# Kernel optimization log

Measured on AMD Instinct MI355X. Metric: run time of the kernel, lower is better.

## Reference

```python
import jax, jax.numpy as jnp
import numpy as np

B, S, DM, NH, DK, DFF = 4, 2048, 512, 8, 64, 2048
EPS = 1e-5


def setup_inputs() -> dict:
    key = jax.random.key(0)
    ks = jax.random.split(key, 16)
    sd = 1.0 / np.sqrt(DM)
    inp = {
        'x': jax.random.normal(ks[0], (B, S, DM), dtype=jnp.float32),
        'wq': jax.random.normal(ks[1], (DM, DM), dtype=jnp.float32) * sd,
        'bq': jnp.zeros((DM,), dtype=jnp.float32),
        'wk': jax.random.normal(ks[2], (DM, DM), dtype=jnp.float32) * sd,
        'bk': jnp.zeros((DM,), dtype=jnp.float32),
        'wv': jax.random.normal(ks[3], (DM, DM), dtype=jnp.float32) * sd,
        'bv': jnp.zeros((DM,), dtype=jnp.float32),
        'wo': jax.random.normal(ks[4], (DM, DM), dtype=jnp.float32) * sd,
        'bo': jnp.zeros((DM,), dtype=jnp.float32),
        'ln_g': jnp.ones((DM,), dtype=jnp.float32),
        'ln_b': jnp.zeros((DM,), dtype=jnp.float32),
        'w1': jax.random.normal(ks[5], (DFF, DM), dtype=jnp.float32) * sd,
        'b1': jnp.zeros((DFF,), dtype=jnp.float32),
        'w2': jax.random.normal(ks[6], (DM, DFF), dtype=jnp.float32) * (1.0 / np.sqrt(DFF)),
        'b2': jnp.zeros((DM,), dtype=jnp.float32),
    }
    return inp


def _layernorm(x, g, b):
    mu = jnp.mean(x, axis=-1, keepdims=True)
    var = jnp.mean(jnp.square(x - mu), axis=-1, keepdims=True)
    return (x - mu) * jax.lax.rsqrt(var + EPS) * g + b


def reference(x, wq, bq, wk, bk, wv, bv, wo, bo, ln_g, ln_b, w1, b1, w2, b2):
    # projections (torch Linear: y = x @ W.T + b)
    q = x @ wq.T + bq
    k = x @ wk.T + bk
    v = x @ wv.T + bv
    # chunk along feature dim into NH heads of size DK
    q = q.reshape(B, S, NH, DK)
    k = k.reshape(B, S, NH, DK)
    v = v.reshape(B, S, NH, DK)
    scores = jnp.einsum('bihd,bjhd->bhij', q, k) / np.sqrt(DK)  # [B,NH,S,S]
    probs = jax.nn.softmax(scores, axis=-1)
    o = jnp.einsum('bhij,bjhd->bihd', probs, v).reshape(B, S, DM)
    o = o @ wo.T + bo
    # residual + shared layernorm (dropout p=0 -> identity)
    h = _layernorm(o + x, ln_g, ln_b)
    ff = jax.nn.relu(h @ w1.T + b1) @ w2.T + b2
    return _layernorm(ff + h, ln_g, ln_b)
```

## Files before the change

### kernel.cpp

```cpp
#include <hip/hip_runtime.h>

typedef __attribute__((ext_vector_type(8))) short short8;
typedef __attribute__((ext_vector_type(8))) unsigned short ushort8;
typedef __attribute__((ext_vector_type(4))) unsigned short ushort4v;
typedef __attribute__((ext_vector_type(4))) float f32x4;
typedef __attribute__((ext_vector_type(16))) float f32x16;

#define DEV static __device__ __forceinline__

DEV unsigned short f2bf(float f) {
  unsigned u = __builtin_bit_cast(unsigned, f);
  u += 0x7fffu + ((u >> 16) & 1u);
  return (unsigned short)(u >> 16);
}

DEV float bf2f(unsigned short u) {
  return __builtin_bit_cast(float, (unsigned)u << 16);
}

DEV void gload_lds16(const void* g, void* l) {
  __builtin_amdgcn_global_load_lds((__attribute__((address_space(1))) void*)g,
                                   (__attribute__((address_space(3))) void*)l,
                                   16, 0, 0);
}

DEV unsigned cvtpk(float lo, float hi) {
  unsigned u;
  asm("v_cvt_pk_bf16_f32 %0, %1, %2" : "=v"(u) : "v"(lo), "v"(hi));
  return u;
}

DEV void pl32(unsigned& a, unsigned& b) {
  asm("v_permlane32_swap_b32 %0, %1" : "+v"(a), "+v"(b));
}

DEV short8 pack4(unsigned a, unsigned b, unsigned c, unsigned d) {
  int4 t = make_int4((int)a, (int)b, (int)c, (int)d);
  return __builtin_bit_cast(short8, t);
}

__global__ __launch_bounds__(256) void cvt_all_k(
    const float4* __restrict__ wq, const float4* __restrict__ wk,
    const float4* __restrict__ wv, const float4* __restrict__ wo,
    const float4* __restrict__ w1, const float4* __restrict__ w2,
    const float4* __restrict__ x, ushort4v* __restrict__ wqkv,
    ushort4v* __restrict__ wob, ushort4v* __restrict__ w1b,
    ushort4v* __restrict__ w2b, ushort4v* __restrict__ xb) {
  const int i = threadIdx.x;
  const int b = blockIdx.x;
  const float4* s;
  ushort4v* d;
  size_t u;
  if (b < 256)       { s = wq; d = wqkv;          u = (size_t)b * 256 + i; }
  else if (b < 512)  { s = wk; d = wqkv + 65536;  u = (size_t)(b - 256) * 256 + i; }
  else if (b < 768)  { s = wv; d = wqkv + 131072; u = (size_t)(b - 512) * 256 + i; }
  else if (b < 1024) { s = wo; d = wob;           u = (size_t)(b - 768) * 256 + i; }
  else if (b < 2048) { s = w1; d = w1b;           u = (size_t)(b - 1024) * 256 + i; }
  else if (b < 3072) { s = w2; d = w2b;           u = (size_t)(b - 2048) * 256 + i; }
  else               { s = x;  d = xb;            u = (size_t)(b - 3072) * 256 + i; }
  float4 v = s[u];
  ushort4v o = { f2bf(v.x), f2bf(v.y), f2bf(v.z), f2bf(v.w) };
  d[u] = o;
}

__global__ void pack_bias_k(const float* __restrict__ bq, const float* __restrict__ bk,
                            const float* __restrict__ bv, float* __restrict__ o) {
  int i = threadIdx.x;
  o[i] = bq[i];
  o[512 + i] = bk[i];
  o[1024 + i] = bv[i];
}

template <int EPI>
__global__ __launch_bounds__(256) void gemm_bt(
    const unsigned short* __restrict__ A, const unsigned short* __restrict__ Bw,
    const float* __restrict__ bias, int M, int N, int K,
    unsigned short* __restrict__ outb, float* __restrict__ outf,
    const unsigned short* __restrict__ residb) {
  __shared__ __align__(16) unsigned short As[128 * 64];
  __shared__ __align__(16) unsigned short Bs[128 * 64];
  const int tid = threadIdx.x;
  const int lane = tid & 63;
  const int wv = tid >> 6;
  const int wr = wv >> 1, wc = wv & 1;
  const int lrow = lane & 15, lgrp = lane >> 4;
  const int bm = blockIdx.x * 128;
  const int bn = blockIdx.y * 128;

  f32x4 acc[4][4];
#pragma unroll
  for (int m = 0; m < 4; m++)
#pragma unroll
    for (int n = 0; n < 4; n++) acc[m][n] = (f32x4){0.f, 0.f, 0.f, 0.f};

  for (int k0 = 0; k0 < K; k0 += 64) {
    __syncthreads();
#pragma unroll
    for (int i = 0; i < 4; i++) {
      const int sb = wv * 64 + i * 256;
      const int slot = sb + lane;
      const int row = slot >> 3;
      const int cc = (slot & 7) ^ (row & 7);
      gload_lds16(A + (size_t)(bm + row) * K + k0 + cc * 8, &As[sb * 8]);
      gload_lds16(Bw + (size_t)(bn + row) * K + k0 + cc * 8, &Bs[sb * 8]);
    }
    __syncthreads();

#pragma unroll
    for (int kk = 0; kk < 2; kk++) {
      short8 af[4], bfr[4];
#pragma unroll
      for (int m = 0; m < 4; m++) {
        const int row = wr * 64 + m * 16 + lrow;
        af[m] = *(const short8*)&As[row * 64 + (((lgrp + 4 * kk) ^ (row & 7)) * 8)];
      }
#pragma unroll
      for (int n = 0; n < 4; n++) {
        const int row = wc * 64 + n * 16 + lrow;
        bfr[n] = *(const short8*)&Bs[row * 64 + (((lgrp + 4 * kk) ^ (row & 7)) * 8)];
      }
#pragma unroll
      for (int m = 0; m < 4; m++)
#pragma unroll
        for (int n = 0; n < 4; n++)
          acc[m][n] = __builtin_amdgcn_mfma_f32_16x16x32_bf16(af[m], bfr[n], acc[m][n], 0, 0, 0);
    }
  }

  if constexpr (EPI == 0) {
    const int proj = bn >> 9;
    if (proj == 2) {
      __shared__ __align__(16) unsigned short VT[128 * 136];
#pragma unroll
      for (int n = 0; n < 4; n++) {
        const int cl = wc * 64 + n * 16 + lrow;
        const float bval = bias[bn + cl];
#pragma unroll
        for (int m = 0; m < 4; m++)
#pragma unroll
          for (int r = 0; r < 4; r++)
            VT[cl * 136 + wr * 64 + m * 16 + lgrp * 4 + r] = f2bf(acc[m][n][r] + bval);
      }
      __syncthreads();
      const int j = (bn - 1024) >> 7;
      const int b = bm >> 11;
      const int sbase = bm & 2047;
      unsigned short* vout = outb + (size_t)2 * 4194304;
#pragma unroll
      for (int q = 0; q < 8; q++) {
        const int chunk = q * 256 + tid;
        const int cl = chunk >> 4, s8 = chunk & 15;
        const int head = 2 * j + (cl >> 6), d = cl & 63;
        ushort8 val = *(const ushort8*)&VT[cl * 136 + s8 * 8];
        *(ushort8*)(vout + ((size_t)(b * 8 + head) * 64 + d) * 2048 + sbase + s8 * 8) = val;
      }
    } else {
      const float qs = (proj == 0) ? 0.18033688011f : 1.0f;
#pragma unroll
      for (int m = 0; m < 4; m++) {
#pragma unroll
        for (int n = 0; n < 4; n++) {
          const int gcol = bn + wc * 64 + n * 16 + lrow;
          const float bval = bias[gcol];
          const int feat = gcol & 511;
          const int head = feat >> 6, d = feat & 63;
#pragma unroll
          for (int r = 0; r < 4; r++) {
            const int grow = bm + wr * 64 + m * 16 + lgrp * 4 + r;
            const int b = grow >> 11, s = grow & 2047;
            const int bh = b * 8 + head;
            outb[(size_t)proj * 4194304 + ((size_t)bh * 2048 + s) * 64 + d] =
                f2bf((acc[m][n][r] + bval) * qs);
          }
        }
      }
    }
  } else {
#pragma unroll
    for (int m = 0; m < 4; m++) {
#pragma unroll
      for (int n = 0; n < 4; n++) {
        const int gcol = bn + wc * 64 + n * 16 + lrow;
        const float bval = bias[gcol];
#pragma unroll
        for (int r = 0; r < 4; r++) {
          const int grow = bm + wr * 64 + m * 16 + lgrp * 4 + r;
          float v = acc[m][n][r] + bval;
          const size_t o = (size_t)grow * N + gcol;
          if constexpr (EPI == 1) {
            outb[o] = f2bf(v + bf2f(residb[o]));
          } else if constexpr (EPI == 2) {
            outb[o] = f2bf(v > 0.f ? v : 0.f);
          } else {
            outf[o] = v + bf2f(residb[o]);
          }
        }
      }
    }
  }
}

template <int EPI>
__global__ __launch_bounds__(256) void gemm_n64(
    const unsigned short* __restrict__ A, const unsigned short* __restrict__ Bw,
    const float* __restrict__ bias, int M, int N, int K,
    unsigned short* __restrict__ outb, float* __restrict__ outf,
    const unsigned short* __restrict__ residb) {
  __shared__ __align__(16) unsigned short As[128 * 64];
  __shared__ __align__(16) unsigned short Bs[64 * 64];
  const int tid = threadIdx.x;
  const int lane = tid & 63;
  const int wv = tid >> 6;
  const int lrow = lane & 15, lgrp = lane >> 4;
  const int bm = blockIdx.x * 128;
  const int bn = blockIdx.y * 64;

  f32x4 acc[2][4];
#pragma unroll
  for (int m = 0; m < 2; m++)
#pragma unroll
    for (int n = 0; n < 4; n++) acc[m][n] = (f32x4){0.f, 0.f, 0.f, 0.f};

  for (int k0 = 0; k0 < K; k0 += 64) {
    __syncthreads();
#pragma unroll
    for (int i = 0; i < 4; i++) {
      const int sb = wv * 64 + i * 256;
      const int slot = sb + lane;
      const int row = slot >> 3;
      const int cc = (slot & 7) ^ (row & 7);
      gload_lds16(A + (size_t)(bm + row) * K + k0 + cc * 8, &As[sb * 8]);
    }
#pragma unroll
    for (int i = 0; i < 2; i++) {
      const int sb = wv * 64 + i * 256;
      const int slot = sb + lane;
      const int row = slot >> 3;
      const int cc = (slot & 7) ^ (row & 7);
      gload_lds16(Bw + (size_t)(bn + row) * K + k0 + cc * 8, &Bs[sb * 8]);
    }
    __syncthreads();

#pragma unroll
    for (int kk = 0; kk < 2; kk++) {
      short8 af[2], bfr[4];
#pragma unroll
      for (int m = 0; m < 2; m++) {
        const int row = wv * 32 + m * 16 + lrow;
        af[m] = *(const short8*)&As[row * 64 + (((lgrp + 4 * kk) ^ (row & 7)) * 8)];
      }
#pragma unroll
      for (int n = 0; n < 4; n++) {
        const int row = n * 16 + lrow;
        bfr[n] = *(const short8*)&Bs[row * 64 + (((lgrp + 4 * kk) ^ (row & 7)) * 8)];
      }
#pragma unroll
      for (int m = 0; m < 2; m++)
#pragma unroll
        for (int n = 0; n < 4; n++)
          acc[m][n] = __builtin_amdgcn_mfma_f32_16x16x32_bf16(af[m], bfr[n], acc[m][n], 0, 0, 0);
    }
  }

#pragma unroll
  for (int m = 0; m < 2; m++) {
#pragma unroll
    for (int n = 0; n < 4; n++) {
      const int gcol = bn + n * 16 + lrow;
      const float bval = bias[gcol];
#pragma unroll
      for (int r = 0; r < 4; r++) {
        const int grow = bm + wv * 32 + m * 16 + lgrp * 4 + r;
        float v = acc[m][n][r] + bval;
        const size_t o = (size_t)grow * N + gcol;
        if constexpr (EPI == 1) {
          outb[o] = f2bf(v + bf2f(residb[o]));
        } else {
          outf[o] = v + bf2f(residb[o]);
        }
      }
    }
  }
}

__global__ __launch_bounds__(256) void attn_k(
    const unsigned short* __restrict__ Qg, const unsigned short* __restrict__ Kg,
    const unsigned short* __restrict__ Vg, unsigned short* __restrict__ Og) {
  __shared__ __align__(16) unsigned short Kl[2][128 * 64];
  __shared__ __align__(16) unsigned short Vl[2][64 * 128];
  const int tid = threadIdx.x, lane = tid & 63, wq = tid >> 6;
  const int ql = lane & 31;
  const int hi = lane >> 5;
  const int bid = blockIdx.x;
  const int lin = (bid & 7) * 64 + (bid >> 3);
  const int bh = lin >> 4;
  const int q0 = (lin & 15) * 128;
  const int qw = q0 + wq * 32;
  const size_t hbase = (size_t)bh * (2048 * 64);

  int kR[4], kC[4], vR[4], vC[4];
#pragma unroll
  for (int i = 0; i < 4; i++) {
    const int slot = i * 256 + tid;
    kR[i] = slot >> 3;
    kC[i] = (slot & 7) ^ (kR[i] & 7);
    vR[i] = slot >> 4;
    vC[i] = (slot & 15) ^ (vR[i] & 15);
  }

  short8 qreg[4];
  {
    const unsigned short* qp = Qg + hbase + (size_t)(qw + ql) * 64 + hi * 8;
#pragma unroll
    for (int i = 0; i < 4; i++) qreg[i] = *(const short8*)(qp + 16 * i);
  }

  f32x16 oac0 = {0.f, 0.f, 0.f, 0.f, 0.f, 0.f, 0.f, 0.f,
                 0.f, 0.f, 0.f, 0.f, 0.f, 0.f, 0.f, 0.f};
  f32x16 oac1 = oac0;
  float lr = 0.f;

#pragma unroll
  for (int i = 0; i < 4; i++) {
    const int db = (i * 256 + wq * 64) * 8;
    gload_lds16(Kg + hbase + (size_t)kR[i] * 64 + kC[i] * 8, &Kl[0][db]);
    gload_lds16(Vg + hbase + (size_t)vR[i] * 2048 + vC[i] * 8, &Vl[0][db]);
  }
  __syncthreads();

  for (int it = 0; it < 16; ++it) {
    const int cur = it & 1;
    if (it < 15) {
      const int kt = (it + 1) * 128;
      const int nxt = cur ^ 1;
#pragma unroll
      for (int i = 0; i < 4; i++) {
        const int db = (i * 256 + wq * 64) * 8;
        gload_lds16(Kg + hbase + (size_t)(kt + kR[i]) * 64 + kC[i] * 8, &Kl[nxt][db]);
        gload_lds16(Vg + hbase + (size_t)vR[i] * 2048 + kt + vC[i] * 8, &Vl[nxt][db]);
      }
    }

#pragma unroll
    for (int hf = 0; hf < 2; hf++) {
      f32x16 sc0 = {0.f, 0.f, 0.f, 0.f, 0.f, 0.f, 0.f, 0.f,
                    0.f, 0.f, 0.f, 0.f, 0.f, 0.f, 0.f, 0.f};
      f32x16 sc1 = sc0;
      __builtin_amdgcn_s_setprio(1);
#pragma unroll
      for (int i = 0; i < 4; i++) {
        const int c8 = 2 * i + hi;
        const int r0 = hf * 64 + ql;
        const int r1 = hf * 64 + ql + 32;
        short8 ka = *(const short8*)&Kl[cur][(r0 * 8 + (c8 ^ (r0 & 7))) * 8];
        short8 kb = *(const short8*)&Kl[cur][(r1 * 8 + (c8 ^ (r1 & 7))) * 8];
        sc0 = __builtin_amdgcn_mfma_f32_32x32x16_bf16(ka, qreg[i], sc0, 0, 0, 0);
        sc1 = __builtin_amdgcn_mfma_f32_32x32x16_bf16(kb, qreg[i], sc1, 0, 0, 0);
      }
      __builtin_amdgcn_s_setprio(0);

      short8 pa[4];
#pragma unroll
      for (int t2 = 0; t2 < 2; t2++) {
        const f32x16& sc = t2 ? sc1 : sc0;
        float p[16];
#pragma unroll
        for (int r = 0; r < 16; r++) {
          p[r] = __builtin_amdgcn_exp2f(sc[r]);
          lr += p[r];
        }
        unsigned w0a = cvtpk(p[0], p[1]),   w0b = cvtpk(p[2], p[3]);
        unsigned w1a = cvtpk(p[4], p[5]),   w1b = cvtpk(p[6], p[7]);
        unsigned w2a = cvtpk(p[8], p[9]),   w2b = cvtpk(p[10], p[11]);
        unsigned w3a = cvtpk(p[12], p[13]), w3b = cvtpk(p[14], p[15]);
        pl32(w0a, w1a);
        pl32(w0b, w1b);
        pa[2 * t2] = pack4(w0a, w0b, w1a, w1b);
        pl32(w2a, w3a);
        pl32(w2b, w3b);
        pa[2 * t2 + 1] = pack4(w2a, w2b, w3a, w3b);
      }

      __builtin_amdgcn_s_setprio(1);
#pragma unroll
      for (int ks = 0; ks < 4; ks++) {
        const int c8 = hf * 8 + 2 * ks + hi;
        const int r0 = ql;
        const int r1 = ql + 32;
        short8 vb0 = *(const short8*)&Vl[cur][(r0 * 16 + (c8 ^ (r0 & 15))) * 8];
        short8 vb1 = *(const short8*)&Vl[cur][(r1 * 16 + (c8 ^ (r1 & 15))) * 8];
        oac0 = __builtin_amdgcn_mfma_f32_32x32x16_bf16(pa[ks], vb0, oac0, 0, 0, 0);
        oac1 = __builtin_amdgcn_mfma_f32_32x32x16_bf16(pa[ks], vb1, oac1, 0, 0, 0);
      }
      __builtin_amdgcn_s_setprio(0);
    }

    __syncthreads();
  }

  lr += __shfl_xor(lr, 32);
  const float inv = 1.0f / lr;

  const int b = bh >> 3, h = bh & 7;
#pragma unroll
  for (int r = 0; r < 16; r++) {
    const int qrow = (r & 3) + 8 * (r >> 2) + 4 * hi;
    const float invr = __shfl(inv, qrow);
    const size_t base = ((size_t)(b * 2048 + qw + qrow)) * 512 + h * 64 + ql;
    Og[base] = f2bf(oac0[r] * invr);
    Og[base + 32] = f2bf(oac1[r] * invr);
  }
}

__global__ __launch_bounds__(64) void ln_k(const float* __restrict__ in,
                                           const float* __restrict__ g,
                                           const float* __restrict__ bb,
                                           float* __restrict__ outf) {
  const int row = blockIdx.x, lane = threadIdx.x;
  const float4* p = (const float4*)(in + (size_t)row * 512);
  float4 a = p[lane], b4 = p[lane + 64];
  float s = a.x + a.y + a.z + a.w + b4.x + b4.y + b4.z + b4.w;
#pragma unroll
  for (int off = 32; off >= 1; off >>= 1) s += __shfl_xor(s, off);
  const float mu = s * (1.f / 512.f);
  float q = 0.f;
  {
    float d;
    d = a.x - mu; q += d * d; d = a.y - mu; q += d * d;
    d = a.z - mu; q += d * d; d = a.w - mu; q += d * d;
    d = b4.x - mu; q += d * d; d = b4.y - mu; q += d * d;
    d = b4.z - mu; q += d * d; d = b4.w - mu; q += d * d;
  }
#pragma unroll
  for (int off = 32; off >= 1; off >>= 1) q += __shfl_xor(q, off);
  const float rstd = rsqrtf(q * (1.f / 512.f) + 1e-5f);
  const float4* gp = (const float4*)g;
  const float4* bp = (const float4*)bb;
  float4 g0 = gp[lane], g1 = gp[lane + 64], c0 = bp[lane], c1 = bp[lane + 64];
  float4 o0, o1;
  o0.x = (a.x - mu) * rstd * g0.x + c0.x;
  o0.y = (a.y - mu) * rstd * g0.y + c0.y;
  o0.z = (a.z - mu) * rstd * g0.z + c0.z;
  o0.w = (a.w - mu) * rstd * g0.w + c0.w;
  o1.x = (b4.x - mu) * rstd * g1.x + c1.x;
  o1.y = (b4.y - mu) * rstd * g1.y + c1.y;
  o1.z = (b4.z - mu) * rstd * g1.z + c1.z;
  o1.w = (b4.w - mu) * rstd * g1.w + c1.w;
  float4* of = (float4*)(outf + (size_t)row * 512);
  of[lane] = o0;
  of[lane + 64] = o1;
}

__global__ __launch_bounds__(64) void ln_bf_k(const unsigned short* __restrict__ in,
                                              const float* __restrict__ g,
                                              const float* __restrict__ bb,
                                              unsigned short* __restrict__ out) {
  const int row = blockIdx.x, lane = threadIdx.x;
  ushort8 v = *(const ushort8*)(in + (size_t)row * 512 + lane * 8);
  float f[8];
#pragma unroll
  for (int j = 0; j < 8; j++) f[j] = bf2f(v[j]);
  float s = 0.f;
#pragma unroll
  for (int j = 0; j < 8; j++) s += f[j];
#pragma unroll
  for (int off = 32; off >= 1; off >>= 1) s += __shfl_xor(s, off);
  const float mu = s * (1.f / 512.f);
  float q = 0.f;
#pragma unroll
  for (int j = 0; j < 8; j++) { const float d = f[j] - mu; q += d * d; }
#pragma unroll
  for (int off = 32; off >= 1; off >>= 1) q += __shfl_xor(q, off);
  const float rstd = rsqrtf(q * (1.f / 512.f) + 1e-5f);
  const float4* gp = (const float4*)g;
  const float4* bp = (const float4*)bb;
  float4 g0 = gp[lane * 2], g1 = gp[lane * 2 + 1];
  float4 c0 = bp[lane * 2], c1 = bp[lane * 2 + 1];
  const float gg[8] = {g0.x, g0.y, g0.z, g0.w, g1.x, g1.y, g1.z, g1.w};
  const float cc[8] = {c0.x, c0.y, c0.z, c0.w, c1.x, c1.y, c1.z, c1.w};
  ushort8 ov;
#pragma unroll
  for (int j = 0; j < 8; j++) ov[j] = f2bf((f[j] - mu) * rstd * gg[j] + cc[j]);
  *(ushort8*)(out + (size_t)row * 512 + lane * 8) = ov;
}

extern "C" void kernel_launch(void* const* d_in, const int* in_sizes, int n_in,
                              void* d_out, int out_size, void* d_ws, size_t ws_size,
                              hipStream_t stream) {
  const float* x = (const float*)d_in[0];
  const float* wq = (const float*)d_in[1];
  const float* bq = (const float*)d_in[2];
  const float* wk = (const float*)d_in[3];
  const float* bk = (const float*)d_in[4];
  const float* wv = (const float*)d_in[5];
  const float* bv = (const float*)d_in[6];
  const float* wo = (const float*)d_in[7];
  const float* bo = (const float*)d_in[8];
  const float* ln_g = (const float*)d_in[9];
  const float* ln_b = (const float*)d_in[10];
  const float* w1 = (const float*)d_in[11];
  const float* b1 = (const float*)d_in[12];
  const float* w2 = (const float*)d_in[13];
  const float* b2 = (const float*)d_in[14];

  unsigned short* ws_u = (unsigned short*)d_ws;
  unsigned short* wqkv = ws_u;
  unsigned short* wob = wqkv + 786432;
  unsigned short* w1b = wob + 262144;
  unsigned short* w2b = w1b + 1048576;
  unsigned short* xb = w2b + 1048576;
  unsigned short* qb = xb + 4194304;
  unsigned short* kb = qb + 4194304;
  unsigned short* vtb = kb + 4194304;
  unsigned short* ob = vtb + 4194304;
  unsigned short* s1b = ob + 4194304;
  unsigned short* hb = s1b + 4194304;
  unsigned short* f1b = qb;
  float* bqkv = (float*)(hb + 4194304);

  cvt_all_k<<<7168, 256, 0, stream>>>(
      (const float4*)wq, (const float4*)wk, (const float4*)wv, (const float4*)wo,
      (const float4*)w1, (const float4*)w2, (const float4*)x,
      (ushort4v*)wqkv, (ushort4v*)wob, (ushort4v*)w1b, (ushort4v*)w2b,
      (ushort4v*)xb);
  pack_bias_k<<<1, 512, 0, stream>>>(bq, bk, bv, bqkv);

  gemm_bt<0><<<dim3(64, 12), 256, 0, stream>>>(xb, wqkv, bqkv, 8192, 1536, 512,
                                               qb, nullptr, nullptr);
  attn_k<<<512, 256, 0, stream>>>(qb, kb, vtb, ob);
  gemm_n64<1><<<dim3(64, 8), 256, 0, stream>>>(ob, wob, bo, 8192, 512, 512,
                                               s1b, nullptr, xb);
  ln_bf_k<<<8192, 64, 0, stream>>>(s1b, ln_g, ln_b, hb);
  gemm_bt<2><<<dim3(64, 16), 256, 0, stream>>>(hb, w1b, b1, 8192, 2048, 512,
                                               f1b, nullptr, nullptr);
  gemm_n64<3><<<dim3(64, 8), 256, 0, stream>>>(f1b, w2b, b2, 8192, 512, 2048,
                                               nullptr, (float*)d_out, hb);
  ln_k<<<8192, 64, 0, stream>>>((float*)d_out, ln_g, ln_b, (float*)d_out);
}
```

Measured before the change: 166.4 us.

## Compute softmax row sums via MFMA and store FFN residual output as bf16

```diff
diff --git a/kernel.cpp b/kernel.cpp
--- a/kernel.cpp
+++ b/kernel.cpp
@@ -315,10 +315,13 @@
     for (int i = 0; i < 4; i++) qreg[i] = *(const short8*)(qp + 16 * i);
   }
 
+  const unsigned one2 = 0x3F803F80u;
+  const short8 ones = pack4(one2, one2, one2, one2);
+
   f32x16 oac0 = {0.f, 0.f, 0.f, 0.f, 0.f, 0.f, 0.f, 0.f,
                  0.f, 0.f, 0.f, 0.f, 0.f, 0.f, 0.f, 0.f};
   f32x16 oac1 = oac0;
-  float lr = 0.f;
+  f32x16 lacc = oac0;
 
 #pragma unroll
   for (int i = 0; i < 4; i++) {
@@ -365,10 +368,7 @@
         const f32x16& sc = t2 ? sc1 : sc0;
         float p[16];
 #pragma unroll
-        for (int r = 0; r < 16; r++) {
-          p[r] = __builtin_amdgcn_exp2f(sc[r]);
-          lr += p[r];
-        }
+        for (int r = 0; r < 16; r++) p[r] = __builtin_amdgcn_exp2f(sc[r]);
         unsigned w0a = cvtpk(p[0], p[1]),   w0b = cvtpk(p[2], p[3]);
         unsigned w1a = cvtpk(p[4], p[5]),   w1b = cvtpk(p[6], p[7]);
         unsigned w2a = cvtpk(p[8], p[9]),   w2b = cvtpk(p[10], p[11]);
@@ -391,64 +391,23 @@
         short8 vb1 = *(const short8*)&Vl[cur][(r1 * 16 + (c8 ^ (r1 & 15))) * 8];
         oac0 = __builtin_amdgcn_mfma_f32_32x32x16_bf16(pa[ks], vb0, oac0, 0, 0, 0);
         oac1 = __builtin_amdgcn_mfma_f32_32x32x16_bf16(pa[ks], vb1, oac1, 0, 0, 0);
+        lacc = __builtin_amdgcn_mfma_f32_32x32x16_bf16(pa[ks], ones, lacc, 0, 0, 0);
       }
       __builtin_amdgcn_s_setprio(0);
     }
 
     __syncthreads();
   }
-
-  lr += __shfl_xor(lr, 32);
-  const float inv = 1.0f / lr;
 
   const int b = bh >> 3, h = bh & 7;
 #pragma unroll
   for (int r = 0; r < 16; r++) {
     const int qrow = (r & 3) + 8 * (r >> 2) + 4 * hi;
-    const float invr = __shfl(inv, qrow);
+    const float invr = 1.0f / lacc[r];
     const size_t base = ((size_t)(b * 2048 + qw + qrow)) * 512 + h * 64 + ql;
     Og[base] = f2bf(oac0[r] * invr);
     Og[base + 32] = f2bf(oac1[r] * invr);
   }
-}
-
-__global__ __launch_bounds__(64) void ln_k(const float* __restrict__ in,
-                                           const float* __restrict__ g,
-                                           const float* __restrict__ bb,
-                                           float* __restrict__ outf) {
-  const int row = blockIdx.x, lane = threadIdx.x;
-  const float4* p = (const float4*)(in + (size_t)row * 512);
-  float4 a = p[lane], b4 = p[lane + 64];
-  float s = a.x + a.y + a.z + a.w + b4.x + b4.y + b4.z + b4.w;
-#pragma unroll
-  for (int off = 32; off >= 1; off >>= 1) s += __shfl_xor(s, off);
-  const float mu = s * (1.f / 512.f);
-  float q = 0.f;
-  {
-    float d;
-    d = a.x - mu; q += d * d; d = a.y - mu; q += d * d;
-    d = a.z - mu; q += d * d; d = a.w - mu; q += d * d;
-    d = b4.x - mu; q += d * d; d = b4.y - mu; q += d * d;
-    d = b4.z - mu; q += d * d; d = b4.w - mu; q += d * d;
-  }
-#pragma unroll
-  for (int off = 32; off >= 1; off >>= 1) q += __shfl_xor(q, off);
-  const float rstd = rsqrtf(q * (1.f / 512.f) + 1e-5f);
-  const float4* gp = (const float4*)g;
-  const float4* bp = (const float4*)bb;
-  float4 g0 = gp[lane], g1 = gp[lane + 64], c0 = bp[lane], c1 = bp[lane + 64];
-  float4 o0, o1;
-  o0.x = (a.x - mu) * rstd * g0.x + c0.x;
-  o0.y = (a.y - mu) * rstd * g0.y + c0.y;
-  o0.z = (a.z - mu) * rstd * g0.z + c0.z;
-  o0.w = (a.w - mu) * rstd * g0.w + c0.w;
-  o1.x = (b4.x - mu) * rstd * g1.x + c1.x;
-  o1.y = (b4.y - mu) * rstd * g1.y + c1.y;
-  o1.z = (b4.z - mu) * rstd * g1.z + c1.z;
-  o1.w = (b4.w - mu) * rstd * g1.w + c1.w;
-  float4* of = (float4*)(outf + (size_t)row * 512);
-  of[lane] = o0;
-  of[lane + 64] = o1;
 }
 
 __global__ __launch_bounds__(64) void ln_bf_k(const unsigned short* __restrict__ in,
@@ -482,6 +441,45 @@
 #pragma unroll
   for (int j = 0; j < 8; j++) ov[j] = f2bf((f[j] - mu) * rstd * gg[j] + cc[j]);
   *(ushort8*)(out + (size_t)row * 512 + lane * 8) = ov;
+}
+
+__global__ __launch_bounds__(64) void ln_bf2f_k(const unsigned short* __restrict__ in,
+                                                const float* __restrict__ g,
+                                                const float* __restrict__ bb,
+                                                float* __restrict__ outf) {
+  const int row = blockIdx.x, lane = threadIdx.x;
+  ushort8 v = *(const ushort8*)(in + (size_t)row * 512 + lane * 8);
+  float f[8];
+#pragma unroll
+  for (int j = 0; j < 8; j++) f[j] = bf2f(v[j]);
+  float s = 0.f;
+#pragma unroll
+  for (int j = 0; j < 8; j++) s += f[j];
+#pragma unroll
+  for (int off = 32; off >= 1; off >>= 1) s += __shfl_xor(s, off);
+  const float mu = s * (1.f / 512.f);
+  float q = 0.f;
+#pragma unroll
+  for (int j = 0; j < 8; j++) { const float d = f[j] - mu; q += d * d; }
+#pragma unroll
+  for (int off = 32; off >= 1; off >>= 1) q += __shfl_xor(q, off);
+  const float rstd = rsqrtf(q * (1.f / 512.f) + 1e-5f);
+  const float4* gp = (const float4*)g;
+  const float4* bp = (const float4*)bb;
+  float4 g0 = gp[lane * 2], g1 = gp[lane * 2 + 1];
+  float4 c0 = bp[lane * 2], c1 = bp[lane * 2 + 1];
+  const float gg[8] = {g0.x, g0.y, g0.z, g0.w, g1.x, g1.y, g1.z, g1.w};
+  const float cc[8] = {c0.x, c0.y, c0.z, c0.w, c1.x, c1.y, c1.z, c1.w};
+  float4 o0, o1;
+  float* o0p = &o0.x;
+  float* o1p = &o1.x;
+#pragma unroll
+  for (int j = 0; j < 4; j++) o0p[j] = (f[j] - mu) * rstd * gg[j] + cc[j];
+#pragma unroll
+  for (int j = 0; j < 4; j++) o1p[j] = (f[j + 4] - mu) * rstd * gg[j + 4] + cc[j + 4];
+  float4* of = (float4*)(outf + (size_t)row * 512 + lane * 8);
+  of[0] = o0;
+  of[1] = o1;
 }
 
 extern "C" void kernel_launch(void* const* d_in, const int* in_sizes, int n_in,
@@ -533,7 +531,7 @@
   ln_bf_k<<<8192, 64, 0, stream>>>(s1b, ln_g, ln_b, hb);
   gemm_bt<2><<<dim3(64, 16), 256, 0, stream>>>(hb, w1b, b1, 8192, 2048, 512,
                                                f1b, nullptr, nullptr);
-  gemm_n64<3><<<dim3(64, 8), 256, 0, stream>>>(f1b, w2b, b2, 8192, 512, 2048,
-                                               nullptr, (float*)d_out, hb);
-  ln_k<<<8192, 64, 0, stream>>>((float*)d_out, ln_g, ln_b, (float*)d_out);
-}
+  gemm_n64<1><<<dim3(64, 8), 256, 0, stream>>>(f1b, w2b, b2, 8192, 512, 2048,
+                                               s1b, nullptr, hb);
+  ln_bf2f_k<<<8192, 64, 0, stream>>>(s1b, ln_g, ln_b, (float*)d_out);
+}
```

Measured after the change: 165.3 us. Within noise of the previous version (-0.6%).
